# Optimization experiments

Hardware: AMD Instinct MI355X
Metric: run time of the kernel (lower is better)

The kernel has to match this reference:

```python
import jax, jax.numpy as jnp
import numpy as np

HIDDEN = 2048
N_HEADS = 32
HEAD_DIM = HIDDEN // N_HEADS  # 64
SEQ = 2048
BATCH = 1
CHUNK = 256
TOPK = 4
THETA = 10000.0
EPS = 1e-6
NEG = jnp.float32(-1e30)


def setup_inputs() -> dict:
    key = jax.random.key(0)
    ks = jax.random.split(key, 8)
    s = 0.02
    return {
        "hidden_states": jax.random.normal(ks[0], (BATCH, SEQ, HIDDEN), jnp.float32),
        "Wq": jax.random.normal(ks[1], (HIDDEN, HIDDEN), jnp.float32) * s,
        "Wk": jax.random.normal(ks[2], (HIDDEN, HIDDEN), jnp.float32) * s,
        "Wv": jax.random.normal(ks[3], (HIDDEN, HIDDEN), jnp.float32) * s,
        "Wo": jax.random.normal(ks[4], (HIDDEN, HIDDEN), jnp.float32) * s,
        "Wg1": jax.random.normal(ks[5], (HEAD_DIM, HIDDEN), jnp.float32) * s,
        "Wg2": jax.random.normal(ks[6], (HIDDEN, HEAD_DIM), jnp.float32) * s,
        "o_norm_weight": jnp.ones((HEAD_DIM,), jnp.float32),
    }


def _rope(t):
    # t: [B, S, H, D]; non-interleaved (NeoX-style) rotary over full head dim
    D = t.shape[-1]
    pos = jnp.arange(t.shape[1], dtype=jnp.float32)
    inv_freq = 1.0 / (THETA ** (jnp.arange(0, D, 2, dtype=jnp.float32) / D))
    freqs = pos[:, None] * inv_freq[None, :]            # [S, D/2]
    cos = jnp.cos(freqs)[None, :, None, :]
    sin = jnp.sin(freqs)[None, :, None, :]
    t1, t2 = t[..., : D // 2], t[..., D // 2:]
    return jnp.concatenate([t1 * cos - t2 * sin, t1 * sin + t2 * cos], axis=-1)


def reference(hidden_states, Wq, Wk, Wv, Wo, Wg1, Wg2, o_norm_weight):
    B, S, _ = hidden_states.shape
    H, D, C = N_HEADS, HEAD_DIM, CHUNK
    NC = S // C

    q = (hidden_states @ Wq.T).reshape(B, S, H, D)
    k = (hidden_states @ Wk.T).reshape(B, S, H, D)
    v = (hidden_states @ Wv.T).reshape(B, S, H, D)
    q, k = _rope(q), _rope(k)

    # --- MoBA gating: per-chunk mean-pooled keys scored against each query ---
    kmean = k.reshape(B, NC, C, H, D).mean(axis=2)           # [B, NC, H, D]
    gate = jnp.einsum('bshd,bnhd->bhsn', q, kmean)           # [B, H, S, NC]

    pos = jnp.arange(S)
    q_chunk = pos // C                                       # [S]
    chunk_ids = jnp.arange(NC)
    future = chunk_ids[None, :] > q_chunk[:, None]           # [S, NC]
    self_blk = chunk_ids[None, :] == q_chunk[:, None]
    gate = jnp.where(future[None, None], NEG, gate)
    gate = jnp.where(self_blk[None, None], -NEG, gate)       # self block always selected

    _, topk_idx = jax.lax.top_k(gate, TOPK)                  # [B, H, S, TOPK]
    sel = jax.nn.one_hot(topk_idx, NC, dtype=jnp.bool_).any(axis=-2)  # [B, H, S, NC]

    # --- block-sparse causal attention over selected chunks ---
    allowed = jnp.take(sel, q_chunk, axis=-1)                # [B, H, S, S] key j -> chunk j//C
    causal = pos[None, :] <= pos[:, None]                    # [S, S]
    allowed = allowed & causal[None, None]

    scale = 1.0 / np.sqrt(D)
    scores = jnp.einsum('bshd,bthd->bhst', q, k) * scale
    scores = jnp.where(allowed, scores, NEG)
    p = jax.nn.softmax(scores, axis=-1)
    o = jnp.einsum('bhst,bthd->bshd', p, v)                  # [B, S, H, D]

    # --- gated RMSNorm (FusedRMSNormGated, sigmoid activation) ---
    g = ((hidden_states @ Wg1.T) @ Wg2.T).reshape(B, S, H, D)
    rms = jax.lax.rsqrt(jnp.mean(o * o, axis=-1, keepdims=True) + EPS)
    o = o * rms * o_norm_weight * jax.nn.sigmoid(g)

    return (o.reshape(B, S, H * D)) @ Wo.T
```

## Files before the change

### kernel.cpp

```cpp
#include <hip/hip_runtime.h>
#include <hip/hip_bf16.h>


typedef __attribute__((ext_vector_type(8))) short s8v;
typedef __attribute__((ext_vector_type(4))) float f4v;

#define MFMA16(A,B,C) __builtin_amdgcn_mfma_f32_16x16x32_bf16(A,B,C,0,0,0)

__device__ __forceinline__ unsigned short f2b_rne(float f){
  unsigned u = __builtin_bit_cast(unsigned, f);
  u = (u + 0x7FFFu + ((u>>16)&1u)) >> 16;
  return (unsigned short)u;
}
__device__ __forceinline__ float b2f(unsigned short h){
  unsigned u = ((unsigned)h)<<16;
  return __builtin_bit_cast(float, u);
}
__device__ __forceinline__ unsigned pack2(float a, float b){
  return (unsigned)f2b_rne(a) | ((unsigned)f2b_rne(b)<<16);
}
__device__ __forceinline__ void gld16(const void* g, void* l){
  __builtin_amdgcn_global_load_lds((const __attribute__((address_space(1))) void*)g,
                                   (__attribute__((address_space(3))) void*)l, 16, 0, 0);
}

__global__ __launch_bounds__(256) void rtab_k(double2* __restrict__ tab){
  const int i = blockIdx.x*256 + threadIdx.x;
  if (i >= 2048*32) return;
  const int d2 = i & 31, s = i >> 5;
  const double invf = 1.0 / pow(10000.0, (double)d2 / 32.0);
  const double ph = (double)s * invf;
  tab[i] = make_double2(cos(ph), sin(ph));
}

__global__ __launch_bounds__(256) void f2b4_k(const float* __restrict__ s,
                                              unsigned short* __restrict__ d, int n4){
  int i = blockIdx.x*256 + threadIdx.x;
  if (i >= n4) return;
  const float4 v = *(const float4*)(s + (size_t)i*4);
  uint2 p; p.x = pack2(v.x, v.y); p.y = pack2(v.z, v.w);
  *(uint2*)(d + (size_t)i*4) = p;
}

__global__ __launch_bounds__(256) void f2bs_k(const float* __restrict__ s,
    unsigned short* __restrict__ hi, unsigned short* __restrict__ lo, int n4){
  int i = blockIdx.x*256 + threadIdx.x;
  if (i >= n4) return;
  const float4 v = *(const float4*)(s + (size_t)i*4);
  unsigned short h0 = f2b_rne(v.x), h1 = f2b_rne(v.y), h2 = f2b_rne(v.z), h3 = f2b_rne(v.w);
  uint2 ph; ph.x = (unsigned)h0 | ((unsigned)h1<<16); ph.y = (unsigned)h2 | ((unsigned)h3<<16);
  uint2 pl; pl.x = pack2(v.x - b2f(h0), v.y - b2f(h1));
  pl.y = pack2(v.z - b2f(h2), v.w - b2f(h3));
  *(uint2*)(hi + (size_t)i*4) = ph;
  *(uint2*)(lo + (size_t)i*4) = pl;
}

__global__ __launch_bounds__(256) void wsum_k(const float* __restrict__ hs,
    const double2* __restrict__ tab, double* __restrict__ Ac, double* __restrict__ As){
  const int n = blockIdx.x, d2 = blockIdx.y, tid = threadIdx.x;
  double ac[8] = {}, as_[8] = {};
  for (int i = 0; i < 256; ++i) {
    const int s = n*256 + i;
    const double2 t = tab[s*32 + d2];
    #pragma unroll
    for (int j = 0; j < 8; ++j) {
      const double v = (double)hs[(size_t)s*2048 + j*256 + tid];
      ac[j] += t.x*v; as_[j] += t.y*v;
    }
  }
  const size_t ro = (size_t)(n*32 + d2)*2048;
  #pragma unroll
  for (int j = 0; j < 8; ++j) {
    Ac[ro + j*256 + tid] = ac[j]*(1.0/256.0);
    As[ro + j*256 + tid] = as_[j]*(1.0/256.0);
  }
}

__global__ __launch_bounds__(64) void kmean2_k(const double* __restrict__ Ac,
    const double* __restrict__ As, const float* __restrict__ Wk,
    double* __restrict__ Km){
  const int n = blockIdx.x, h = blockIdx.y, d = threadIdx.x;
  const int d2 = d & 31;
  const bool hiHalf = d >= 32;
  const float* wk1 = Wk + (size_t)(h*64 + d2)*2048;
  const float* wk2 = Wk + (size_t)(h*64 + d2 + 32)*2048;
  const double* ac = Ac + (size_t)(n*32 + d2)*2048;
  const double* as_ = As + (size_t)(n*32 + d2)*2048;
  double a = 0.0, b = 0.0;
  for (int c = 0; c < 2048; ++c) {
    if (!hiHalf) { a += ac[c]*(double)wk1[c]; b += as_[c]*(double)wk2[c]; }
    else         { a += as_[c]*(double)wk1[c]; b += ac[c]*(double)wk2[c]; }
  }
  Km[(size_t)(n*32 + h)*64 + d] = hiHalf ? (a + b) : (a - b);
}

__global__ __launch_bounds__(256) void gate_topk_k(const float* __restrict__ Qf,
    const double* __restrict__ Km, unsigned char* __restrict__ Allow,
    unsigned char* __restrict__ Flags){
  const int h = blockIdx.x, c = blockIdx.y, t = threadIdx.x;
  __shared__ double km[512];
  km[t]     = Km[((t>>6)*32 + h)*64 + (t&63)];
  km[t+256] = Km[(((t+256)>>6)*32 + h)*64 + (t&63)];
  __syncthreads();
  const int s = c*256 + t;
  const float* qp = Qf + (size_t)s*2048 + h*64;
  double g[8] = {};
  for (int d = 0; d < 64; ++d) {
    const double qv = (double)qp[d];
    #pragma unroll
    for (int n2 = 0; n2 < 8; ++n2) g[n2] += qv*km[n2*64+d];
  }
  double margin = 1e300;
  if (c >= 4) {
    unsigned pm = 0;
    double v[4];
    for (int rep = 0; rep < 4; ++rep) {
      double best = -1e308; int bi = 0;
      #pragma unroll
      for (int n2 = 0; n2 < 8; ++n2) {
        const bool take = (n2 < c) && !((pm>>n2)&1u) && (g[n2] > best);
        best = take ? g[n2] : best;
        bi   = take ? n2 : bi;
      }
      v[rep] = best; pm |= 1u<<bi;
    }
    margin = v[2] - v[3];
  }
  Flags[h*2048 + s] = (margin < 1e-3) ? 1 : 0;
  #pragma unroll
  for (int n2 = 0; n2 < 8; ++n2) if (n2 > c) g[n2] = -1e300;
  g[c] = 1e300;
  unsigned mask = 0;
  for (int rep = 0; rep < 4; ++rep) {
    double best = -1e308; int bi = 0;
    #pragma unroll
    for (int n2 = 0; n2 < 8; ++n2) {
      const bool take = !((mask>>n2)&1u) && (g[n2] > best);
      best = take ? g[n2] : best;
      bi   = take ? n2 : bi;
    }
    mask |= 1u<<bi;
  }
  Allow[h*2048 + s] = (unsigned char)mask;
}

__global__ __launch_bounds__(64) void repair_k(
    const float* __restrict__ hs, const float* __restrict__ Wq,
    const double2* __restrict__ tab, const double* __restrict__ Km,
    const unsigned char* __restrict__ Flags, unsigned char* __restrict__ Allow)
{
  const int s = blockIdx.x, d = threadIdx.x;
  __shared__ double qr[64];
  __shared__ double g8[8];
  for (int h = 0; h < 32; ++h) {
    if (!Flags[h*2048 + s]) continue;
    const float* hrow = hs + (size_t)s*2048;
    const float* wrow = Wq + (size_t)(h*64 + d)*2048;
    double a0=0,a1=0,a2=0,a3=0;
    for (int k = 0; k < 2048; k += 4) {
      a0 += (double)hrow[k]  *(double)wrow[k];
      a1 += (double)hrow[k+1]*(double)wrow[k+1];
      a2 += (double)hrow[k+2]*(double)wrow[k+2];
      a3 += (double)hrow[k+3]*(double)wrow[k+3];
    }
    qr[d] = (a0+a1)+(a2+a3);
    __syncthreads();
    const double2 t = tab[s*32 + (d&31)];
    const double rot = (d < 32) ? (qr[d]*t.x - qr[d+32]*t.y)
                                : (qr[d-32]*t.y + qr[d]*t.x);
    __syncthreads();
    qr[d] = rot;
    __syncthreads();
    if (d < 8) {
      double g = 0;
      const double* kmp = Km + (size_t)(d*32 + h)*64;
      for (int dd = 0; dd < 64; ++dd) g += qr[dd]*kmp[dd];
      g8[d] = g;
    }
    __syncthreads();
    if (d == 0) {
      const int c = s >> 8;
      double g[8];
      #pragma unroll
      for (int n2 = 0; n2 < 8; ++n2)
        g[n2] = (n2 > c) ? -1e300 : ((n2 == c) ? 1e300 : g8[n2]);
      unsigned mask = 0;
      for (int rep = 0; rep < 4; ++rep) {
        double best = -1e308; int bi = 0;
        #pragma unroll
        for (int n2 = 0; n2 < 8; ++n2) {
          const bool take = !((mask>>n2)&1u) && (g[n2] > best);
          best = take ? g[n2] : best;
          bi   = take ? n2 : bi;
        }
        mask |= 1u<<bi;
      }
      Allow[h*2048 + s] = (unsigned char)mask;
    }
    __syncthreads();
  }
}

__global__ __launch_bounds__(256) void gemm4_bt(
    const unsigned short* __restrict__ Ah, const unsigned short* __restrict__ Al,
    const unsigned short* __restrict__ Bh0, const unsigned short* __restrict__ Bl0,
    const unsigned short* __restrict__ Bh1, const unsigned short* __restrict__ Bl1,
    const unsigned short* __restrict__ Bh2, const unsigned short* __restrict__ Bl2,
    float* __restrict__ C0, float* __restrict__ C1, float* __restrict__ C2,
    int M, int N, int K)
{
  alignas(16) __shared__ char SAh[16384];
  alignas(16) __shared__ char SAl[16384];
  alignas(16) __shared__ char SBh[16384];
  alignas(16) __shared__ char SBl[16384];
  const int z = blockIdx.z;
  const unsigned short* Bh = (z==0) ? Bh0 : ((z==1) ? Bh1 : Bh2);
  const unsigned short* Bl = (z==0) ? Bl0 : ((z==1) ? Bl1 : Bl2);
  float* C = (z==0) ? C0 : ((z==1) ? C1 : C2);
  const int t = threadIdx.x;
  const int wave = t>>6, lane = t&63, lg = lane>>4, lr = lane&15;
  const int wm = wave >> 1, wn = wave & 1;
  const int m0 = blockIdx.x*128, n0 = blockIdx.y*128;
  const unsigned short* Ahb = Ah + (size_t)m0*K;
  const unsigned short* Alb = Al + (size_t)m0*K;
  const unsigned short* Bhb = Bh + (size_t)n0*K;
  const unsigned short* Blb = Bl + (size_t)n0*K;
  f4v acc[4][4] = {};
  #pragma unroll 1
  for (int kt = 0; kt < K; kt += 64) {
    __syncthreads();
    #pragma unroll
    for (int i = 0; i < 4; ++i) {
      const size_t go = (size_t)(i*32 + (t>>3))*K + kt + (t&7)*8;
      gld16(Ahb + go, SAh + i*4096 + wave*1024);
      gld16(Alb + go, SAl + i*4096 + wave*1024);
      gld16(Bhb + go, SBh + i*4096 + wave*1024);
      gld16(Blb + go, SBl + i*4096 + wave*1024);
    }
    __syncthreads();
    #pragma unroll
    for (int kk = 0; kk < 2; ++kk) {
      s8v ah[4], al[4], bh[4], bl[4];
      #pragma unroll
      for (int i = 0; i < 4; ++i) {
        const int ro = (wm*64 + i*16 + lr)*128 + kk*64 + lg*16;
        ah[i] = *(const s8v*)&SAh[ro];
        al[i] = *(const s8v*)&SAl[ro];
      }
      #pragma unroll
      for (int j = 0; j < 4; ++j) {
        const int ro = (wn*64 + j*16 + lr)*128 + kk*64 + lg*16;
        bh[j] = *(const s8v*)&SBh[ro];
        bl[j] = *(const s8v*)&SBl[ro];
      }
      #pragma unroll
      for (int i = 0; i < 4; ++i)
        #pragma unroll
        for (int j = 0; j < 4; ++j) {
          f4v a = acc[i][j];
          a = MFMA16(ah[i], bh[j], a);
          a = MFMA16(ah[i], bl[j], a);
          a = MFMA16(al[i], bh[j], a);
          a = MFMA16(al[i], bl[j], a);
          acc[i][j] = a;
        }
    }
  }
  #pragma unroll
  for (int i = 0; i < 4; ++i)
    #pragma unroll
    for (int j = 0; j < 4; ++j) {
      const int row = m0 + wm*64 + i*16 + lg*4;
      const int col = n0 + wn*64 + j*16 + lr;
      #pragma unroll
      for (int r = 0; r < 4; ++r)
        C[(size_t)(row+r)*N + col] = acc[i][j][r];
    }
}

template<int BM, int BN, int WN, bool OUTBF>
__global__ __launch_bounds__(256) void gemm_bt(
    const unsigned short* __restrict__ A, const unsigned short* __restrict__ B,
    void* __restrict__ C, int M, int N, int K)
{
  alignas(16) __shared__ char AsB[BM*128];
  alignas(16) __shared__ char BsB[BN*128];
  const int t = threadIdx.x;
  const int wave = t>>6, lane = t&63, lg = lane>>4, lr = lane&15;
  const int wm = wave / WN, wn = wave % WN;
  const int m0 = blockIdx.x*BM, n0 = blockIdx.y*BN;
  const unsigned short* Ab = A + (size_t)m0*K;
  const unsigned short* Bb = B + (size_t)n0*K;
  f4v acc[4][4] = {};
  #pragma unroll 1
  for (int kt = 0; kt < K; kt += 64) {
    __syncthreads();
    #pragma unroll
    for (int i = 0; i < BM/32; ++i)
      gld16(Ab + (size_t)(i*32 + (t>>3))*K + kt + (t&7)*8, AsB + i*4096 + wave*1024);
    #pragma unroll
    for (int i = 0; i < BN/32; ++i)
      gld16(Bb + (size_t)(i*32 + (t>>3))*K + kt + (t&7)*8, BsB + i*4096 + wave*1024);
    __syncthreads();
    #pragma unroll
    for (int kk = 0; kk < 2; ++kk) {
      s8v af[4], bfr[4];
      #pragma unroll
      for (int i = 0; i < 4; ++i)
        af[i] = *(const s8v*)&AsB[(wm*64 + i*16 + lr)*128 + kk*64 + lg*16];
      #pragma unroll
      for (int j = 0; j < 4; ++j)
        bfr[j] = *(const s8v*)&BsB[(wn*64 + j*16 + lr)*128 + kk*64 + lg*16];
      #pragma unroll
      for (int i = 0; i < 4; ++i)
        #pragma unroll
        for (int j = 0; j < 4; ++j)
          acc[i][j] = MFMA16(af[i], bfr[j], acc[i][j]);
    }
  }
  #pragma unroll
  for (int i = 0; i < 4; ++i)
    #pragma unroll
    for (int j = 0; j < 4; ++j) {
      const int row = m0 + wm*64 + i*16 + lg*4;
      const int col = n0 + wn*64 + j*16 + lr;
      #pragma unroll
      for (int r = 0; r < 4; ++r) {
        if (OUTBF) ((unsigned short*)C)[(size_t)(row+r)*N + col] = f2b_rne(acc[i][j][r]);
        else       ((float*)C)[(size_t)(row+r)*N + col] = acc[i][j][r];
      }
    }
}

__global__ __launch_bounds__(256) void rope32q_k(float* __restrict__ Qf,
    unsigned short* __restrict__ Qb, const double2* __restrict__ tab){
  const int idx = blockIdx.x*256 + threadIdx.x;
  const int d2 = idx & 31, hh = (idx>>5)&31, s = idx>>10;
  const double2 t = tab[s*32 + d2];
  const float cs = (float)t.x, sn = (float)t.y;
  const size_t base = (size_t)s*2048 + hh*64 + d2;
  const float q1 = Qf[base], q2 = Qf[base+32];
  const float o1 = q1*cs - q2*sn, o2 = q1*sn + q2*cs;
  Qf[base] = o1; Qf[base+32] = o2;
  Qb[base] = f2b_rne(o1); Qb[base+32] = f2b_rne(o2);
}

__global__ __launch_bounds__(256) void rope32_k(const float* __restrict__ Kf,
    unsigned short* __restrict__ Kb, const double2* __restrict__ tab){
  const int idx = blockIdx.x*256 + threadIdx.x;
  const int d2 = idx & 31, hh = (idx>>5)&31, s = idx>>10;
  const double2 t = tab[s*32 + d2];
  const float cs = (float)t.x, sn = (float)t.y;
  const size_t base = (size_t)s*2048 + hh*64 + d2;
  const float k1 = Kf[base], k2 = Kf[base+32];
  Kb[base]    = f2b_rne(k1*cs - k2*sn);
  Kb[base+32] = f2b_rne(k1*sn + k2*cs);
}

__global__ __launch_bounds__(256) void vtrans_k(const float* __restrict__ V,
                                                unsigned short* __restrict__ Vt){
  __shared__ unsigned short tile[64][68];
  const int s0 = blockIdx.x*64, c0 = blockIdx.y*64;
  const int tx = threadIdx.x & 63, ty = threadIdx.x >> 6;
  #pragma unroll
  for (int rr = 0; rr < 16; ++rr) {
    const int r = ty*16 + rr;
    tile[tx][r] = f2b_rne(V[(size_t)(s0+r)*2048 + c0+tx]);
  }
  __syncthreads();
  #pragma unroll
  for (int rr = 0; rr < 16; ++rr) {
    const int cc = ty*16 + rr;
    Vt[(size_t)(c0+cc)*2048 + s0+tx] = tile[cc][tx];
  }
}

__global__ __launch_bounds__(64) void attn_k(
    const unsigned short* __restrict__ Qb, const unsigned short* __restrict__ Kb,
    const unsigned short* __restrict__ Vt, const float* __restrict__ Gf,
    const unsigned char* __restrict__ Allow, const float* __restrict__ Wn,
    float* __restrict__ Of)
{
  const int h = blockIdx.x, c = blockIdx.y, zb = blockIdx.z;
  const int lane = threadIdx.x, lg = lane>>4, lr = lane&15;
  const int qbase = c*256 + zb*64;
  alignas(16) __shared__ char P[8192];

  s8v qf[4][2];
  unsigned am[4];
  #pragma unroll
  for (int jq = 0; jq < 4; ++jq) {
    const size_t qrow = (size_t)(qbase + jq*16 + lr);
    qf[jq][0] = *(const s8v*)&Qb[qrow*2048 + h*64 + lg*8];
    qf[jq][1] = *(const s8v*)&Qb[qrow*2048 + h*64 + 32 + lg*8];
    am[jq] = Allow[h*2048 + qrow];
  }
  float mx[4] = {-1e30f,-1e30f,-1e30f,-1e30f};
  float ls[4] = {0,0,0,0};
  f4v ot[4][4] = {};
  const unsigned amAll = am[0]|am[1]|am[2]|am[3];

  for (int n = 0; n <= c; ++n) {
    if (!__ballot((amAll>>n)&1u)) continue;
    #pragma unroll 1
    for (int t4 = 0; t4 < 4; ++t4) {
      const int kb0 = n*256 + t4*64;
      s8v kf[4][2];
      #pragma unroll
      for (int i = 0; i < 4; ++i) {
        const size_t krow = (size_t)(kb0 + i*16 + lr);
        kf[i][0] = *(const s8v*)&Kb[krow*2048 + h*64 + lg*8];
        kf[i][1] = *(const s8v*)&Kb[krow*2048 + h*64 + 32 + lg*8];
      }
      f4v st[4][4];
      #pragma unroll
      for (int i = 0; i < 4; ++i)
        #pragma unroll
        for (int jq = 0; jq < 4; ++jq) {
          f4v zz = {};
          zz = MFMA16(kf[i][0], qf[jq][0], zz);
          st[i][jq] = MFMA16(kf[i][1], qf[jq][1], zz);
        }
      float cm[4] = {-__builtin_inff(),-__builtin_inff(),-__builtin_inff(),-__builtin_inff()};
      #pragma unroll
      for (int jq = 0; jq < 4; ++jq) {
        const int okc = (am[jq]>>n)&1;
        const int q = qbase + jq*16 + lr;
        #pragma unroll
        for (int i = 0; i < 4; ++i)
          #pragma unroll
          for (int r = 0; r < 4; ++r) {
            float v = st[i][jq][r]*0.125f;
            const int key = kb0 + i*16 + lg*4 + r;
            const bool ok = okc && (n != c || key <= q);
            v = ok ? v : -__builtin_inff();
            st[i][jq][r] = v;
            cm[jq] = fmaxf(cm[jq], v);
          }
      }
      #pragma unroll
      for (int jq = 0; jq < 4; ++jq) {
        cm[jq] = fmaxf(cm[jq], __shfl_xor(cm[jq], 16));
        cm[jq] = fmaxf(cm[jq], __shfl_xor(cm[jq], 32));
      }
      float al[4];
      #pragma unroll
      for (int jq = 0; jq < 4; ++jq) {
        const float nm = fmaxf(mx[jq], cm[jq]);
        al[jq] = __expf(mx[jq] - nm);
        mx[jq] = nm;
      }
      float ps[4] = {0,0,0,0};
      #pragma unroll
      for (int jq = 0; jq < 4; ++jq) {
        const int q = jq*16 + lr;
        const int sw = (q&7)<<4;
        #pragma unroll
        for (int i = 0; i < 4; ++i) {
          const float p0 = __expf(st[i][jq][0]-mx[jq]);
          const float p1 = __expf(st[i][jq][1]-mx[jq]);
          const float p2 = __expf(st[i][jq][2]-mx[jq]);
          const float p3 = __expf(st[i][jq][3]-mx[jq]);
          ps[jq] += (p0+p1)+(p2+p3);
          uint2 pk; pk.x = pack2(p0,p1); pk.y = pack2(p2,p3);
          *(uint2*)&P[q*128 + ((i*32 + lg*8) ^ sw)] = pk;
        }
      }
      #pragma unroll
      for (int jq = 0; jq < 4; ++jq) {
        ps[jq] += __shfl_xor(ps[jq], 16);
        ps[jq] += __shfl_xor(ps[jq], 32);
        ls[jq] = ls[jq]*al[jq] + ps[jq];
      }
      #pragma unroll
      for (int jd = 0; jd < 4; ++jd)
        #pragma unroll
        for (int jq = 0; jq < 4; ++jq)
          ot[jd][jq] *= al[jq];
      asm volatile("s_waitcnt lgkmcnt(0)" ::: "memory");
      __builtin_amdgcn_sched_barrier(0);
      #pragma unroll
      for (int kk = 0; kk < 2; ++kk) {
        s8v vfr[4], pfr[4];
        #pragma unroll
        for (int jd = 0; jd < 4; ++jd)
          vfr[jd] = *(const s8v*)&Vt[(size_t)(h*64 + jd*16 + lr)*2048 + kb0 + kk*32 + lg*8];
        #pragma unroll
        for (int jq = 0; jq < 4; ++jq) {
          const int q = jq*16 + lr;
          pfr[jq] = *(const s8v*)&P[q*128 + ((kk*64 + lg*16) ^ ((q&7)<<4))];
        }
        #pragma unroll
        for (int jd = 0; jd < 4; ++jd)
          #pragma unroll
          for (int jq = 0; jq < 4; ++jq)
            ot[jd][jq] = MFMA16(vfr[jd], pfr[jq], ot[jd][jq]);
      }
      asm volatile("s_waitcnt lgkmcnt(0)" ::: "memory");
      __builtin_amdgcn_sched_barrier(0);
    }
  }
  float inv_[4], ssum[4] = {0,0,0,0}, rmsv[4];
  #pragma unroll
  for (int jq = 0; jq < 4; ++jq) inv_[jq] = 1.0f/ls[jq];
  #pragma unroll
  for (int jd = 0; jd < 4; ++jd)
    #pragma unroll
    for (int jq = 0; jq < 4; ++jq)
      #pragma unroll
      for (int r = 0; r < 4; ++r) {
        const float o = ot[jd][jq][r]*inv_[jq];
        ot[jd][jq][r] = o;
        ssum[jq] += o*o;
      }
  #pragma unroll
  for (int jq = 0; jq < 4; ++jq) {
    float s2 = ssum[jq];
    s2 += __shfl_xor(s2, 16);
    s2 += __shfl_xor(s2, 32);
    rmsv[jq] = rsqrtf(s2*(1.0f/64.0f) + 1e-6f);
  }
  float wv[4][4];
  #pragma unroll
  for (int jd = 0; jd < 4; ++jd) {
    const float4 w4 = *(const float4*)&Wn[jd*16 + lg*4];
    wv[jd][0]=w4.x; wv[jd][1]=w4.y; wv[jd][2]=w4.z; wv[jd][3]=w4.w;
  }
  #pragma unroll
  for (int jq = 0; jq < 4; ++jq) {
    const size_t q = (size_t)(qbase + jq*16 + lr);
    #pragma unroll
    for (int jd = 0; jd < 4; ++jd) {
      const float4 g4 = *(const float4*)&Gf[q*2048 + h*64 + jd*16 + lg*4];
      float4 o4;
      o4.x = ot[jd][jq][0]*rmsv[jq]*wv[jd][0]*(1.0f/(1.0f+__expf(-g4.x)));
      o4.y = ot[jd][jq][1]*rmsv[jq]*wv[jd][1]*(1.0f/(1.0f+__expf(-g4.y)));
      o4.z = ot[jd][jq][2]*rmsv[jq]*wv[jd][2]*(1.0f/(1.0f+__expf(-g4.z)));
      o4.w = ot[jd][jq][3]*rmsv[jq]*wv[jd][3]*(1.0f/(1.0f+__expf(-g4.w)));
      *(float4*)&Of[q*2048 + h*64 + jd*16 + lg*4] = o4;
    }
  }
}

extern "C" void kernel_launch(void* const* d_in, const int* in_sizes, int n_in,
                              void* d_out, int out_size, void* d_ws, size_t ws_size,
                              hipStream_t stream)
{
  const float* hs  = (const float*)d_in[0];
  const float* Wq  = (const float*)d_in[1];
  const float* Wk  = (const float*)d_in[2];
  const float* Wv  = (const float*)d_in[3];
  const float* Wo  = (const float*)d_in[4];
  const float* Wg1 = (const float*)d_in[5];
  const float* Wg2 = (const float*)d_in[6];
  const float* Wn  = (const float*)d_in[7];

  const size_t S2 = (size_t)2048*2048;
  const size_t MB = (size_t)1<<20;
  char* ws = (char*)d_ws;
  double2*        tab   = (double2*)       (ws);
  unsigned short* hsh   = (unsigned short*)(ws + 1*MB);
  unsigned short* hsl   = (unsigned short*)(ws + 9*MB);
  unsigned short* Wqh   = (unsigned short*)(ws + 17*MB);
  unsigned short* Wql   = (unsigned short*)(ws + 25*MB);
  unsigned short* Wkh   = (unsigned short*)(ws + 33*MB);
  unsigned short* Wkl   = (unsigned short*)(ws + 41*MB);
  unsigned short* Wvh   = (unsigned short*)(ws + 49*MB);
  unsigned short* Wvl   = (unsigned short*)(ws + 57*MB);
  unsigned short* Wg1b  = (unsigned short*)(ws + 65*MB);
  unsigned short* Wg2b  = (unsigned short*)(ws + 65*MB + 262144);
  unsigned short* g1b   = (unsigned short*)(ws + 65*MB + 524288);
  double*         km    = (double*)        (ws + 65*MB + 786432);
  unsigned char*  allow = (unsigned char*) (ws + 65*MB + 917504);
  unsigned char*  flags = (unsigned char*) (ws + 65*MB + 983040);
  float*          qf    = (float*)         (ws + 66*MB);
  float*          kf    = (float*)         (ws + 82*MB);
  float*          vf    = (float*)         (ws + 98*MB);
  unsigned short* qb    = (unsigned short*)(ws + 17*MB);
  unsigned short* kb    = (unsigned short*)(ws + 25*MB);
  double*         Ac    = (double*)        (ws + 57*MB);
  double*         As    = (double*)        (ws + 61*MB);
  unsigned short* vt    = (unsigned short*)(ws + 82*MB);
  float*          gf    = (float*)         (ws + 98*MB);
  float*          of    = (float*)         (ws + 33*MB);
  unsigned short* ofb   = (unsigned short*)(ws + 90*MB);
  unsigned short* Wob   = (unsigned short*)(ws + 66*MB);
  (void)ws_size; (void)in_sizes; (void)n_in; (void)out_size;

  rtab_k<<<256,256,0,stream>>>(tab);
  f2bs_k<<<4096,256,0,stream>>>(hs, hsh, hsl, (int)(S2/4));
  f2bs_k<<<4096,256,0,stream>>>(Wq, Wqh, Wql, (int)(S2/4));
  f2bs_k<<<4096,256,0,stream>>>(Wk, Wkh, Wkl, (int)(S2/4));
  f2bs_k<<<4096,256,0,stream>>>(Wv, Wvh, Wvl, (int)(S2/4));
  f2b4_k<<<128,256,0,stream>>>(Wg1, Wg1b, 64*2048/4);
  f2b4_k<<<128,256,0,stream>>>(Wg2, Wg2b, 2048*64/4);

  gemm4_bt<<<dim3(16,16,3),256,0,stream>>>(hsh, hsl, Wqh, Wql, Wkh, Wkl, Wvh, Wvl,
                                           qf, kf, vf, 2048, 2048, 2048);
  rope32q_k<<<8192,256,0,stream>>>(qf, qb, tab);
  rope32_k<<<8192,256,0,stream>>>(kf, kb, tab);
  vtrans_k<<<dim3(32,32),256,0,stream>>>(vf, vt);

  wsum_k<<<dim3(8,32),256,0,stream>>>(hs, tab, Ac, As);
  kmean2_k<<<dim3(8,32),64,0,stream>>>(Ac, As, Wk, km);
  gate_topk_k<<<dim3(32,8),256,0,stream>>>(qf, km, allow, flags);
  repair_k<<<2048,64,0,stream>>>(hs, Wq, tab, km, flags, allow);

  gemm_bt<256,64,1,true><<<dim3(8,1),256,0,stream>>>(hsh, Wg1b, g1b, 2048, 64, 2048);
  gemm_bt<128,128,2,false><<<dim3(16,16),256,0,stream>>>(g1b, Wg2b, gf, 2048, 2048, 64);

  attn_k<<<dim3(32,8,4),64,0,stream>>>(qb, kb, vt, gf, allow, Wn, of);

  f2b4_k<<<4096,256,0,stream>>>(of, ofb, (int)(S2/4));
  f2b4_k<<<4096,256,0,stream>>>(Wo, Wob, (int)(S2/4));
  gemm_bt<128,128,2,false><<<dim3(16,16),256,0,stream>>>(ofb, Wob, d_out, 2048, 2048, 2048);
}
```

Baseline: 862.9 us.

## Use single bf16 for K/V projections, shrink attention tiles, split kmean reduction

The K and V projections drop the split-bf16 hi/lo (roughly 4-pass) GEMM and use a plain bf16 GEMM, which cuts MFMA work and weight conversion traffic for two of the three projections. Only Q keeps the higher-precision split GEMM. The attention kernel now handles 16 queries per wave instead of 64, giving 4x more blocks for occupancy but reloading K and V more often per query. kmean2 spreads its 2048-length reduction over 4 waves with a shared-memory combine. The lower K/V precision could affect top-k chunk selection and accuracy.

```diff
diff --git a/kernel.cpp b/kernel.cpp
--- a/kernel.cpp
+++ b/kernel.cpp
@@ -76,10 +76,11 @@
   }
 }
 
-__global__ __launch_bounds__(64) void kmean2_k(const double* __restrict__ Ac,
+__global__ __launch_bounds__(256) void kmean2_k(const double* __restrict__ Ac,
     const double* __restrict__ As, const float* __restrict__ Wk,
     double* __restrict__ Km){
-  const int n = blockIdx.x, h = blockIdx.y, d = threadIdx.x;
+  const int n = blockIdx.x, h = blockIdx.y;
+  const int tid = threadIdx.x, d = tid & 63, p = tid >> 6;
   const int d2 = d & 31;
   const bool hiHalf = d >= 32;
   const float* wk1 = Wk + (size_t)(h*64 + d2)*2048;
@@ -87,11 +88,15 @@
   const double* ac = Ac + (size_t)(n*32 + d2)*2048;
   const double* as_ = As + (size_t)(n*32 + d2)*2048;
   double a = 0.0, b = 0.0;
-  for (int c = 0; c < 2048; ++c) {
+  for (int c = p*512; c < p*512 + 512; ++c) {
     if (!hiHalf) { a += ac[c]*(double)wk1[c]; b += as_[c]*(double)wk2[c]; }
     else         { a += as_[c]*(double)wk1[c]; b += ac[c]*(double)wk2[c]; }
   }
-  Km[(size_t)(n*32 + h)*64 + d] = hiHalf ? (a + b) : (a - b);
+  __shared__ double red[256];
+  red[tid] = hiHalf ? (a + b) : (a - b);
+  __syncthreads();
+  if (p == 0)
+    Km[(size_t)(n*32 + h)*64 + d] = (red[d] + red[d+64]) + (red[d+128] + red[d+192]);
 }
 
 __global__ __launch_bounds__(256) void gate_topk_k(const float* __restrict__ Qf,
@@ -203,20 +208,13 @@
 
 __global__ __launch_bounds__(256) void gemm4_bt(
     const unsigned short* __restrict__ Ah, const unsigned short* __restrict__ Al,
-    const unsigned short* __restrict__ Bh0, const unsigned short* __restrict__ Bl0,
-    const unsigned short* __restrict__ Bh1, const unsigned short* __restrict__ Bl1,
-    const unsigned short* __restrict__ Bh2, const unsigned short* __restrict__ Bl2,
-    float* __restrict__ C0, float* __restrict__ C1, float* __restrict__ C2,
-    int M, int N, int K)
+    const unsigned short* __restrict__ Bh, const unsigned short* __restrict__ Bl,
+    float* __restrict__ C, int M, int N, int K)
 {
   alignas(16) __shared__ char SAh[16384];
   alignas(16) __shared__ char SAl[16384];
   alignas(16) __shared__ char SBh[16384];
   alignas(16) __shared__ char SBl[16384];
-  const int z = blockIdx.z;
-  const unsigned short* Bh = (z==0) ? Bh0 : ((z==1) ? Bh1 : Bh2);
-  const unsigned short* Bl = (z==0) ? Bl0 : ((z==1) ? Bl1 : Bl2);
-  float* C = (z==0) ? C0 : ((z==1) ? C1 : C2);
   const int t = threadIdx.x;
   const int wave = t>>6, lane = t&63, lg = lane>>4, lr = lane&15;
   const int wm = wave >> 1, wn = wave & 1;
@@ -383,25 +381,22 @@
 {
   const int h = blockIdx.x, c = blockIdx.y, zb = blockIdx.z;
   const int lane = threadIdx.x, lg = lane>>4, lr = lane&15;
-  const int qbase = c*256 + zb*64;
-  alignas(16) __shared__ char P[8192];
-
-  s8v qf[4][2];
-  unsigned am[4];
-  #pragma unroll
-  for (int jq = 0; jq < 4; ++jq) {
-    const size_t qrow = (size_t)(qbase + jq*16 + lr);
-    qf[jq][0] = *(const s8v*)&Qb[qrow*2048 + h*64 + lg*8];
-    qf[jq][1] = *(const s8v*)&Qb[qrow*2048 + h*64 + 32 + lg*8];
-    am[jq] = Allow[h*2048 + qrow];
-  }
-  float mx[4] = {-1e30f,-1e30f,-1e30f,-1e30f};
-  float ls[4] = {0,0,0,0};
-  f4v ot[4][4] = {};
-  const unsigned amAll = am[0]|am[1]|am[2]|am[3];
+  const int qbase = c*256 + zb*16;
+  alignas(16) __shared__ char P[2048];
+
+  const size_t qrow = (size_t)(qbase + lr);
+  const s8v qf0 = *(const s8v*)&Qb[qrow*2048 + h*64 + lg*8];
+  const s8v qf1 = *(const s8v*)&Qb[qrow*2048 + h*64 + 32 + lg*8];
+  const unsigned am = Allow[h*2048 + qrow];
+  const int q = qbase + lr;
+  const int sw = (lr&7)<<4;
+
+  float mx = -1e30f, ls = 0.f;
+  f4v ot[4] = {};
 
   for (int n = 0; n <= c; ++n) {
-    if (!__ballot((amAll>>n)&1u)) continue;
+    if (!__ballot((am>>n)&1u)) continue;
+    const int okc = (am>>n)&1;
     #pragma unroll 1
     for (int t4 = 0; t4 < 4; ++t4) {
       const int kb0 = n*256 + t4*64;
@@ -412,133 +407,86 @@
         kf[i][0] = *(const s8v*)&Kb[krow*2048 + h*64 + lg*8];
         kf[i][1] = *(const s8v*)&Kb[krow*2048 + h*64 + 32 + lg*8];
       }
-      f4v st[4][4];
+      f4v st[4];
+      #pragma unroll
+      for (int i = 0; i < 4; ++i) {
+        f4v zz = {};
+        zz = MFMA16(kf[i][0], qf0, zz);
+        st[i] = MFMA16(kf[i][1], qf1, zz);
+      }
+      float cm = -__builtin_inff();
       #pragma unroll
       for (int i = 0; i < 4; ++i)
         #pragma unroll
-        for (int jq = 0; jq < 4; ++jq) {
-          f4v zz = {};
-          zz = MFMA16(kf[i][0], qf[jq][0], zz);
-          st[i][jq] = MFMA16(kf[i][1], qf[jq][1], zz);
+        for (int r = 0; r < 4; ++r) {
+          float v = st[i][r]*0.125f;
+          const int key = kb0 + i*16 + lg*4 + r;
+          const bool ok = okc && (n != c || key <= q);
+          v = ok ? v : -__builtin_inff();
+          st[i][r] = v;
+          cm = fmaxf(cm, v);
         }
-      float cm[4] = {-__builtin_inff(),-__builtin_inff(),-__builtin_inff(),-__builtin_inff()};
-      #pragma unroll
-      for (int jq = 0; jq < 4; ++jq) {
-        const int okc = (am[jq]>>n)&1;
-        const int q = qbase + jq*16 + lr;
-        #pragma unroll
-        for (int i = 0; i < 4; ++i)
-          #pragma unroll
-          for (int r = 0; r < 4; ++r) {
-            float v = st[i][jq][r]*0.125f;
-            const int key = kb0 + i*16 + lg*4 + r;
-            const bool ok = okc && (n != c || key <= q);
-            v = ok ? v : -__builtin_inff();
-            st[i][jq][r] = v;
-            cm[jq] = fmaxf(cm[jq], v);
-          }
-      }
-      #pragma unroll
-      for (int jq = 0; jq < 4; ++jq) {
-        cm[jq] = fmaxf(cm[jq], __shfl_xor(cm[jq], 16));
-        cm[jq] = fmaxf(cm[jq], __shfl_xor(cm[jq], 32));
-      }
-      float al[4];
-      #pragma unroll
-      for (int jq = 0; jq < 4; ++jq) {
-        const float nm = fmaxf(mx[jq], cm[jq]);
-        al[jq] = __expf(mx[jq] - nm);
-        mx[jq] = nm;
-      }
-      float ps[4] = {0,0,0,0};
-      #pragma unroll
-      for (int jq = 0; jq < 4; ++jq) {
-        const int q = jq*16 + lr;
-        const int sw = (q&7)<<4;
-        #pragma unroll
-        for (int i = 0; i < 4; ++i) {
-          const float p0 = __expf(st[i][jq][0]-mx[jq]);
-          const float p1 = __expf(st[i][jq][1]-mx[jq]);
-          const float p2 = __expf(st[i][jq][2]-mx[jq]);
-          const float p3 = __expf(st[i][jq][3]-mx[jq]);
-          ps[jq] += (p0+p1)+(p2+p3);
-          uint2 pk; pk.x = pack2(p0,p1); pk.y = pack2(p2,p3);
-          *(uint2*)&P[q*128 + ((i*32 + lg*8) ^ sw)] = pk;
-        }
-      }
-      #pragma unroll
-      for (int jq = 0; jq < 4; ++jq) {
-        ps[jq] += __shfl_xor(ps[jq], 16);
-        ps[jq] += __shfl_xor(ps[jq], 32);
-        ls[jq] = ls[jq]*al[jq] + ps[jq];
-      }
-      #pragma unroll
-      for (int jd = 0; jd < 4; ++jd)
-        #pragma unroll
-        for (int jq = 0; jq < 4; ++jq)
-          ot[jd][jq] *= al[jq];
+      cm = fmaxf(cm, __shfl_xor(cm, 16));
+      cm = fmaxf(cm, __shfl_xor(cm, 32));
+      const float nm = fmaxf(mx, cm);
+      const float al = __expf(mx - nm);
+      mx = nm;
+      float ps = 0.f;
+      #pragma unroll
+      for (int i = 0; i < 4; ++i) {
+        const float p0 = __expf(st[i][0]-mx);
+        const float p1 = __expf(st[i][1]-mx);
+        const float p2 = __expf(st[i][2]-mx);
+        const float p3 = __expf(st[i][3]-mx);
+        ps += (p0+p1)+(p2+p3);
+        uint2 pk; pk.x = pack2(p0,p1); pk.y = pack2(p2,p3);
+        *(uint2*)&P[lr*128 + ((i*32 + lg*8) ^ sw)] = pk;
+      }
+      ps += __shfl_xor(ps, 16);
+      ps += __shfl_xor(ps, 32);
+      ls = ls*al + ps;
+      #pragma unroll
+      for (int jd = 0; jd < 4; ++jd) ot[jd] *= al;
       asm volatile("s_waitcnt lgkmcnt(0)" ::: "memory");
       __builtin_amdgcn_sched_barrier(0);
       #pragma unroll
       for (int kk = 0; kk < 2; ++kk) {
-        s8v vfr[4], pfr[4];
+        s8v vfr[4];
         #pragma unroll
         for (int jd = 0; jd < 4; ++jd)
           vfr[jd] = *(const s8v*)&Vt[(size_t)(h*64 + jd*16 + lr)*2048 + kb0 + kk*32 + lg*8];
-        #pragma unroll
-        for (int jq = 0; jq < 4; ++jq) {
-          const int q = jq*16 + lr;
-          pfr[jq] = *(const s8v*)&P[q*128 + ((kk*64 + lg*16) ^ ((q&7)<<4))];
-        }
+        const s8v pfr = *(const s8v*)&P[lr*128 + ((kk*64 + lg*16) ^ sw)];
         #pragma unroll
         for (int jd = 0; jd < 4; ++jd)
-          #pragma unroll
-          for (int jq = 0; jq < 4; ++jq)
-            ot[jd][jq] = MFMA16(vfr[jd], pfr[jq], ot[jd][jq]);
+          ot[jd] = MFMA16(vfr[jd], pfr, ot[jd]);
       }
       asm volatile("s_waitcnt lgkmcnt(0)" ::: "memory");
       __builtin_amdgcn_sched_barrier(0);
     }
   }
-  float inv_[4], ssum[4] = {0,0,0,0}, rmsv[4];
-  #pragma unroll
-  for (int jq = 0; jq < 4; ++jq) inv_[jq] = 1.0f/ls[jq];
+  const float inv_ = 1.0f/ls;
+  float ssum = 0.f;
   #pragma unroll
   for (int jd = 0; jd < 4; ++jd)
     #pragma unroll
-    for (int jq = 0; jq < 4; ++jq)
-      #pragma unroll
-      for (int r = 0; r < 4; ++r) {
-        const float o = ot[jd][jq][r]*inv_[jq];
-        ot[jd][jq][r] = o;
-        ssum[jq] += o*o;
-      }
-  #pragma unroll
-  for (int jq = 0; jq < 4; ++jq) {
-    float s2 = ssum[jq];
-    s2 += __shfl_xor(s2, 16);
-    s2 += __shfl_xor(s2, 32);
-    rmsv[jq] = rsqrtf(s2*(1.0f/64.0f) + 1e-6f);
-  }
-  float wv[4][4];
+    for (int r = 0; r < 4; ++r) {
+      const float o = ot[jd][r]*inv_;
+      ot[jd][r] = o;
+      ssum += o*o;
+    }
+  ssum += __shfl_xor(ssum, 16);
+  ssum += __shfl_xor(ssum, 32);
+  const float rmsv = rsqrtf(ssum*(1.0f/64.0f) + 1e-6f);
   #pragma unroll
   for (int jd = 0; jd < 4; ++jd) {
     const float4 w4 = *(const float4*)&Wn[jd*16 + lg*4];
-    wv[jd][0]=w4.x; wv[jd][1]=w4.y; wv[jd][2]=w4.z; wv[jd][3]=w4.w;
-  }
-  #pragma unroll
-  for (int jq = 0; jq < 4; ++jq) {
-    const size_t q = (size_t)(qbase + jq*16 + lr);
-    #pragma unroll
-    for (int jd = 0; jd < 4; ++jd) {
-      const float4 g4 = *(const float4*)&Gf[q*2048 + h*64 + jd*16 + lg*4];
-      float4 o4;
-      o4.x = ot[jd][jq][0]*rmsv[jq]*wv[jd][0]*(1.0f/(1.0f+__expf(-g4.x)));
-      o4.y = ot[jd][jq][1]*rmsv[jq]*wv[jd][1]*(1.0f/(1.0f+__expf(-g4.y)));
-      o4.z = ot[jd][jq][2]*rmsv[jq]*wv[jd][2]*(1.0f/(1.0f+__expf(-g4.z)));
-      o4.w = ot[jd][jq][3]*rmsv[jq]*wv[jd][3]*(1.0f/(1.0f+__expf(-g4.w)));
-      *(float4*)&Of[q*2048 + h*64 + jd*16 + lg*4] = o4;
-    }
+    const float4 g4 = *(const float4*)&Gf[qrow*2048 + h*64 + jd*16 + lg*4];
+    float4 o4;
+    o4.x = ot[jd][0]*rmsv*w4.x*(1.0f/(1.0f+__expf(-g4.x)));
+    o4.y = ot[jd][1]*rmsv*w4.y*(1.0f/(1.0f+__expf(-g4.y)));
+    o4.z = ot[jd][2]*rmsv*w4.z*(1.0f/(1.0f+__expf(-g4.z)));
+    o4.w = ot[jd][3]*rmsv*w4.w*(1.0f/(1.0f+__expf(-g4.w)));
+    *(float4*)&Of[qrow*2048 + h*64 + jd*16 + lg*4] = o4;
   }
 }
 
@@ -563,53 +511,53 @@
   unsigned short* hsl   = (unsigned short*)(ws + 9*MB);
   unsigned short* Wqh   = (unsigned short*)(ws + 17*MB);
   unsigned short* Wql   = (unsigned short*)(ws + 25*MB);
-  unsigned short* Wkh   = (unsigned short*)(ws + 33*MB);
-  unsigned short* Wkl   = (unsigned short*)(ws + 41*MB);
-  unsigned short* Wvh   = (unsigned short*)(ws + 49*MB);
-  unsigned short* Wvl   = (unsigned short*)(ws + 57*MB);
-  unsigned short* Wg1b  = (unsigned short*)(ws + 65*MB);
-  unsigned short* Wg2b  = (unsigned short*)(ws + 65*MB + 262144);
-  unsigned short* g1b   = (unsigned short*)(ws + 65*MB + 524288);
-  double*         km    = (double*)        (ws + 65*MB + 786432);
-  unsigned char*  allow = (unsigned char*) (ws + 65*MB + 917504);
-  unsigned char*  flags = (unsigned char*) (ws + 65*MB + 983040);
-  float*          qf    = (float*)         (ws + 66*MB);
-  float*          kf    = (float*)         (ws + 82*MB);
-  float*          vf    = (float*)         (ws + 98*MB);
-  unsigned short* qb    = (unsigned short*)(ws + 17*MB);
-  unsigned short* kb    = (unsigned short*)(ws + 25*MB);
-  double*         Ac    = (double*)        (ws + 57*MB);
-  double*         As    = (double*)        (ws + 61*MB);
-  unsigned short* vt    = (unsigned short*)(ws + 82*MB);
-  float*          gf    = (float*)         (ws + 98*MB);
+  unsigned short* Wkb   = (unsigned short*)(ws + 33*MB);
+  unsigned short* Wvb   = (unsigned short*)(ws + 41*MB);
+  unsigned short* Wg1b  = (unsigned short*)(ws + 49*MB);
+  unsigned short* Wg2b  = (unsigned short*)(ws + 49*MB + 262144);
+  unsigned short* g1b   = (unsigned short*)(ws + 49*MB + 524288);
+  double*         km    = (double*)        (ws + 49*MB + 786432);
+  unsigned char*  allow = (unsigned char*) (ws + 49*MB + 917504);
+  unsigned char*  flags = (unsigned char*) (ws + 49*MB + 983040);
+  float*          qf    = (float*)         (ws + 50*MB);
+  float*          kf    = (float*)         (ws + 66*MB);
+  float*          vf    = (float*)         (ws + 82*MB);
+  double*         Ac    = (double*)        (ws + 98*MB);
+  double*         As    = (double*)        (ws + 102*MB);
+  unsigned short* kb    = (unsigned short*)(ws + 17*MB);
+  unsigned short* qb    = (unsigned short*)(ws + 25*MB);
+  unsigned short* vt    = (unsigned short*)(ws + 66*MB);
+  unsigned short* ofb   = (unsigned short*)(ws + 74*MB);
+  float*          gf    = (float*)         (ws + 82*MB);
   float*          of    = (float*)         (ws + 33*MB);
-  unsigned short* ofb   = (unsigned short*)(ws + 90*MB);
-  unsigned short* Wob   = (unsigned short*)(ws + 66*MB);
+  unsigned short* Wob   = (unsigned short*)(ws + 50*MB);
   (void)ws_size; (void)in_sizes; (void)n_in; (void)out_size;
 
   rtab_k<<<256,256,0,stream>>>(tab);
   f2bs_k<<<4096,256,0,stream>>>(hs, hsh, hsl, (int)(S2/4));
   f2bs_k<<<4096,256,0,stream>>>(Wq, Wqh, Wql, (int)(S2/4));
-  f2bs_k<<<4096,256,0,stream>>>(Wk, Wkh, Wkl, (int)(S2/4));
-  f2bs_k<<<4096,256,0,stream>>>(Wv, Wvh, Wvl, (int)(S2/4));
+  f2b4_k<<<4096,256,0,stream>>>(Wk, Wkb, (int)(S2/4));
+  f2b4_k<<<4096,256,0,stream>>>(Wv, Wvb, (int)(S2/4));
   f2b4_k<<<128,256,0,stream>>>(Wg1, Wg1b, 64*2048/4);
   f2b4_k<<<128,256,0,stream>>>(Wg2, Wg2b, 2048*64/4);
 
-  gemm4_bt<<<dim3(16,16,3),256,0,stream>>>(hsh, hsl, Wqh, Wql, Wkh, Wkl, Wvh, Wvl,
-                                           qf, kf, vf, 2048, 2048, 2048);
+  gemm4_bt<<<dim3(16,16),256,0,stream>>>(hsh, hsl, Wqh, Wql, qf, 2048, 2048, 2048);
+  gemm_bt<128,128,2,false><<<dim3(16,16),256,0,stream>>>(hsh, Wkb, kf, 2048, 2048, 2048);
+  gemm_bt<128,128,2,false><<<dim3(16,16),256,0,stream>>>(hsh, Wvb, vf, 2048, 2048, 2048);
+
   rope32q_k<<<8192,256,0,stream>>>(qf, qb, tab);
   rope32_k<<<8192,256,0,stream>>>(kf, kb, tab);
   vtrans_k<<<dim3(32,32),256,0,stream>>>(vf, vt);
 
   wsum_k<<<dim3(8,32),256,0,stream>>>(hs, tab, Ac, As);
-  kmean2_k<<<dim3(8,32),64,0,stream>>>(Ac, As, Wk, km);
+  kmean2_k<<<dim3(8,32),256,0,stream>>>(Ac, As, Wk, km);
   gate_topk_k<<<dim3(32,8),256,0,stream>>>(qf, km, allow, flags);
   repair_k<<<2048,64,0,stream>>>(hs, Wq, tab, km, flags, allow);
 
   gemm_bt<256,64,1,true><<<dim3(8,1),256,0,stream>>>(hsh, Wg1b, g1b, 2048, 64, 2048);
   gemm_bt<128,128,2,false><<<dim3(16,16),256,0,stream>>>(g1b, Wg2b, gf, 2048, 2048, 64);
 
-  attn_k<<<dim3(32,8,4),64,0,stream>>>(qb, kb, vt, gf, allow, Wn, of);
+  attn_k<<<dim3(32,8,16),64,0,stream>>>(qb, kb, vt, gf, allow, Wn, of);
 
   f2b4_k<<<4096,256,0,stream>>>(of, ofb, (int)(S2/4));
   f2b4_k<<<4096,256,0,stream>>>(Wo, Wob, (int)(S2/4));
```

Result: slower. 965.9 us (+11.9%).
